# Kernel tuning notes

Measured on AMD Instinct MI355X. Metric: run time of the kernel, lower is better.

## Reference

```python
import jax, jax.numpy as jnp
import numpy as np

EPS = 1e-5


def _lstm_agg(x, nbr_idx, Wih, Whh, bih, bhh):
    # x: [N, D] node feats; nbr_idx: [N, K]; LSTM hidden size == D (DGL lstm aggregator)
    seq = x[nbr_idx]                     # [N, K, D] irregular gather
    N, K, D = seq.shape
    seq_t = jnp.swapaxes(seq, 0, 1)      # [K, N, D] time-major for scan

    def step(carry, xt):
        h, c = carry
        z = xt @ Wih.T + bih + h @ Whh.T + bhh   # [N, 4D]; torch gate order i,f,g,o
        i, f, g, o = jnp.split(z, 4, axis=-1)
        i = jax.nn.sigmoid(i)
        f = jax.nn.sigmoid(f)
        g = jnp.tanh(g)
        o = jax.nn.sigmoid(o)
        c = f * c + i * g
        h = o * jnp.tanh(c)
        return (h, c), None

    zero = jnp.zeros((N, D), seq.dtype)
    (h, _), _ = jax.lax.scan(step, (zero, zero), seq_t)
    return h                             # final hidden state = neighbor aggregate


def _sage_layer(x, nbr_idx, Wih, Whh, bih, bhh, Wself, bself, Wneigh):
    h_neigh = _lstm_agg(x, nbr_idx, Wih, Whh, bih, bhh)
    return x @ Wself.T + bself + h_neigh @ Wneigh.T


def _bn(x, gamma, beta):
    # BatchNorm1d in training mode: batch statistics over the node axis
    mu = jnp.mean(x, axis=0)
    var = jnp.var(x, axis=0)
    return (x - mu) * jax.lax.rsqrt(var + EPS) * gamma + beta


def setup_inputs() -> dict:
    key = jax.random.key(0)
    N, K, D_IN, D_H = 100000, 16, 128, 128
    ks = jax.random.split(key, 20)
    s = 0.05
    inp = {
        "in_feat": jax.random.normal(ks[0], (N, D_IN), jnp.float32),
        "nbr_idx": jax.random.randint(ks[1], (N, K), 0, N, jnp.int32),
        # layer 1 (in_feats=128 -> h_feats=128), LSTM hidden = in_feats
        "Wih1": jax.random.normal(ks[2], (4 * D_IN, D_IN), jnp.float32) * s,
        "Whh1": jax.random.normal(ks[3], (4 * D_IN, D_IN), jnp.float32) * s,
        "bih1": jnp.zeros((4 * D_IN,), jnp.float32),
        "bhh1": jnp.zeros((4 * D_IN,), jnp.float32),
        "Wself1": jax.random.normal(ks[4], (D_H, D_IN), jnp.float32) * s,
        "bself1": jnp.zeros((D_H,), jnp.float32),
        "Wneigh1": jax.random.normal(ks[5], (D_H, D_IN), jnp.float32) * s,
        "gamma1": jnp.ones((D_H,), jnp.float32),
        "beta1": jnp.zeros((D_H,), jnp.float32),
        # layer 2 (h_feats=128 -> h_feats=128)
        "Wih2": jax.random.normal(ks[6], (4 * D_H, D_H), jnp.float32) * s,
        "Whh2": jax.random.normal(ks[7], (4 * D_H, D_H), jnp.float32) * s,
        "bih2": jnp.zeros((4 * D_H,), jnp.float32),
        "bhh2": jnp.zeros((4 * D_H,), jnp.float32),
        "Wself2": jax.random.normal(ks[8], (D_H, D_H), jnp.float32) * s,
        "bself2": jnp.zeros((D_H,), jnp.float32),
        "Wneigh2": jax.random.normal(ks[9], (D_H, D_H), jnp.float32) * s,
        "gamma2": jnp.ones((D_H,), jnp.float32),
        "beta2": jnp.zeros((D_H,), jnp.float32),
    }
    return inp


def reference(in_feat, nbr_idx,
              Wih1, Whh1, bih1, bhh1, Wself1, bself1, Wneigh1, gamma1, beta1,
              Wih2, Whh2, bih2, bhh2, Wself2, bself2, Wneigh2, gamma2, beta2):
    h = _sage_layer(in_feat, nbr_idx, Wih1, Whh1, bih1, bhh1, Wself1, bself1, Wneigh1)
    h = jax.nn.relu(_bn(h, gamma1, beta1))
    h = _sage_layer(h, nbr_idx, Wih2, Whh2, bih2, bhh2, Wself2, bself2, Wneigh2)
    h = _bn(h, gamma2, beta2)
    return h
```

## Files before the change

### kernel.cpp

```cpp
#include <hip/hip_runtime.h>

typedef unsigned short u16;
typedef unsigned int u32;
typedef unsigned long long u64;
typedef __attribute__((ext_vector_type(8))) short short8;
typedef __attribute__((ext_vector_type(4))) float float4_t;

__device__ __forceinline__ float bf2f(u16 v) {
    union { u32 u; float f; } x; x.u = ((u32)v) << 16; return x.f;
}
__device__ __forceinline__ u16 f2bf(float f) {
    union { float f; u32 u; } x; x.f = f;
    u32 r = x.u + 0x7FFFu + ((x.u >> 16) & 1u);
    return (u16)(r >> 16);
}
__device__ __forceinline__ u32 pk2bf(float hi, float lo) {
    union { float f; u32 u; } a, b; a.f = hi; b.f = lo;
    return __builtin_amdgcn_perm(a.u + 0x8000u, b.u + 0x8000u, 0x07060302u);
}
#define LOG2E 1.44269504088896340736f
__device__ __forceinline__ float sigm(float x) {
    return __builtin_amdgcn_rcpf(1.f + __builtin_amdgcn_exp2f(-LOG2E * x));
}
__device__ __forceinline__ float tanh_(float x) {
    float t = __builtin_amdgcn_exp2f(2.f * LOG2E * x);
    return 1.f - 2.f * __builtin_amdgcn_rcpf(1.f + t);
}

__device__ __forceinline__ float4_t mfma16(short8 a, short8 b, float4_t c) {
    return __builtin_amdgcn_mfma_f32_16x16x32_bf16(a, b, c, 0, 0, 0);
}

__device__ __forceinline__ short8 ldfrag(const u16* p) { return *(const short8*)p; }
__device__ __forceinline__ short8 ldfrag(const float* p) {
    float4_t a = *(const float4_t*)p;
    float4_t b = *(const float4_t*)(p + 4);
    short8 r;
#pragma unroll
    for (int j = 0; j < 4; ++j) { r[j] = (short)f2bf(a[j]); r[4 + j] = (short)f2bf(b[j]); }
    return r;
}

template<typename AT>
__global__ __launch_bounds__(256) void gemm_ih(
    const AT* __restrict__ A, const float* __restrict__ W,
    const float* __restrict__ b1, const float* __restrict__ b2,
    u16* __restrict__ C, int M)
{
    const int P = 512;
    const int lane = threadIdx.x & 63;
    const int w    = threadIdx.x >> 6;
    const int l15  = lane & 15;
    const int quad = lane >> 4;
    const int rowbase = blockIdx.x * 64;
    const int colbase = blockIdx.y * 128 + w * 32;

    short8 af[4][4];
#pragma unroll
    for (int mb = 0; mb < 4; ++mb) {
        int row = rowbase + mb * 16 + l15;
        if (row >= M) row = M - 1;
        const AT* ap = A + (size_t)row * 128 + quad * 8;
#pragma unroll
        for (int kb = 0; kb < 4; ++kb) af[mb][kb] = ldfrag(ap + kb * 32);
    }
    short8 bfr[2][4];
#pragma unroll
    for (int nb = 0; nb < 2; ++nb) {
        int col = colbase + nb * 16 + l15;
        const float* wp = W + (size_t)col * 128 + quad * 8;
#pragma unroll
        for (int kb = 0; kb < 4; ++kb) bfr[nb][kb] = ldfrag(wp + kb * 32);
    }
    const float4_t z4 = {0.f, 0.f, 0.f, 0.f};
    float bias[2];
#pragma unroll
    for (int nb = 0; nb < 2; ++nb) {
        int col = colbase + nb * 16 + l15;
        bias[nb] = b1[col] + b2[col];
    }
#pragma unroll
    for (int mb = 0; mb < 4; ++mb)
#pragma unroll
        for (int nb = 0; nb < 2; ++nb) {
            float4_t a = z4;
#pragma unroll
            for (int kb = 0; kb < 4; ++kb) a = mfma16(af[mb][kb], bfr[nb][kb], a);
#pragma unroll
            for (int r = 0; r < 4; ++r) {
                int row = rowbase + mb * 16 + quad * 4 + r;
                int col = colbase + nb * 16 + l15;
                if (row < M) C[(size_t)row * P + col] = f2bf(a[r] + bias[nb]);
            }
        }
}

template<typename T>
__device__ __forceinline__ void accum_gemm(
    const T* __restrict__ A, const float* __restrict__ W,
    float4_t (&acc)[4][2], int M, int rowbase, int colbase, int l15, int quad)
{
    short8 af[4][4];
#pragma unroll
    for (int mb = 0; mb < 4; ++mb) {
        int row = rowbase + mb * 16 + l15;
        if (row >= M) row = M - 1;
        const T* ap = A + (size_t)row * 128 + quad * 8;
#pragma unroll
        for (int kb = 0; kb < 4; ++kb) af[mb][kb] = ldfrag(ap + kb * 32);
    }
    short8 bfr[2][4];
#pragma unroll
    for (int nb = 0; nb < 2; ++nb) {
        int col = colbase + nb * 16 + l15;
        const float* wp = W + (size_t)col * 128 + quad * 8;
#pragma unroll
        for (int kb = 0; kb < 4; ++kb) bfr[nb][kb] = ldfrag(wp + kb * 32);
    }
#pragma unroll
    for (int mb = 0; mb < 4; ++mb)
#pragma unroll
        for (int nb = 0; nb < 2; ++nb)
#pragma unroll
            for (int kb = 0; kb < 4; ++kb)
                acc[mb][nb] = mfma16(af[mb][kb], bfr[nb][kb], acc[mb][nb]);
}

template<typename AT2>
__global__ __launch_bounds__(256) void gemm_out(
    const u16* __restrict__ A1, const float* __restrict__ W1,
    const AT2* __restrict__ A2, const float* __restrict__ W2,
    const float* __restrict__ bias, float* __restrict__ C,
    float* __restrict__ stats, int M)
{
    const int P = 128;
    const int lane = threadIdx.x & 63;
    const int w    = threadIdx.x >> 6;
    const int l15  = lane & 15;
    const int quad = lane >> 4;
    const int rowbase = blockIdx.x * 64;
    const int colbase = w * 32;

    float4_t acc[4][2];
    const float4_t z4 = {0.f, 0.f, 0.f, 0.f};
#pragma unroll
    for (int mb = 0; mb < 4; ++mb)
#pragma unroll
        for (int nb = 0; nb < 2; ++nb) acc[mb][nb] = z4;

    accum_gemm(A1, W1, acc, M, rowbase, colbase, l15, quad);
    accum_gemm(A2, W2, acc, M, rowbase, colbase, l15, quad);

    float s[2] = {0.f, 0.f}, sq[2] = {0.f, 0.f};
#pragma unroll
    for (int nb = 0; nb < 2; ++nb) {
        int col = colbase + nb * 16 + l15;
        float bb = bias[col];
#pragma unroll
        for (int mb = 0; mb < 4; ++mb)
#pragma unroll
            for (int r = 0; r < 4; ++r) {
                int row = rowbase + mb * 16 + quad * 4 + r;
                if (row < M) {
                    float v = acc[mb][nb][r] + bb;
                    C[(size_t)row * P + col] = v;
                    s[nb] += v; sq[nb] += v * v;
                }
            }
    }
#pragma unroll
    for (int nb = 0; nb < 2; ++nb) {
        float t1 = s[nb], t2 = sq[nb];
        t1 += __shfl_xor(t1, 16); t1 += __shfl_xor(t1, 32);
        t2 += __shfl_xor(t2, 16); t2 += __shfl_xor(t2, 32);
        int col = colbase + nb * 16 + l15;
        if (quad == 0) atomicAdd(&stats[col], t1);
        if (quad == 1) atomicAdd(&stats[P + col], t2);
    }
}

__global__ __launch_bounds__(512, 2) void lstm_kernel(
    const u16* __restrict__ Xih,
    const int* __restrict__ nbr,
    const float* __restrict__ Whh,
    u16* __restrict__ Hout,
    int N)
{
    __shared__ u16 hbuf[2][64][136];
    __shared__ int nbrs[16][72];
    const int tid  = threadIdx.x;
    const int lane = tid & 63;
    const int w    = tid >> 6;
    const int l15  = lane & 15;
    const int quad = lane >> 4;
    const int base = blockIdx.x * 64;

    short8 whA[4][4];
#pragma unroll
    for (int g = 0; g < 4; ++g) {
        int row = 128 * g + 16 * w + l15;
        const float* wp = Whh + (size_t)row * 128 + quad * 8;
#pragma unroll
        for (int kb = 0; kb < 4; ++kb) whA[g][kb] = ldfrag(wp + kb * 32);
    }
    short8 I;
    {
        int off = (w & 1) ? 16 : 0;
#pragma unroll
        for (int j = 0; j < 8; ++j) {
            int k = quad * 8 + j;
            I[j] = (short)((k == l15 + off) ? 0x3F80 : 0);
        }
    }
    u32* hz = (u32*)&hbuf[0][0][0];
    for (int i = tid; i < 2 * 64 * 136 / 2; i += 512) hz[i] = 0u;
    for (int i = tid; i < 64 * 16; i += 512) {
        int node = base + (i >> 4);
        if (node >= N) node = N - 1;
        nbrs[i & 15][i >> 4] = nbr[(size_t)node * 16 + (i & 15)];
    }
    __syncthreads();

    const int xcol0 = 32 * (w >> 1);
    short8 xf[4][4];
#pragma unroll
    for (int nb = 0; nb < 4; ++nb) {
        int node = nbrs[0][l15 + 16 * nb];
        const u16* xp = Xih + (size_t)node * 512 + xcol0 + quad * 8;
#pragma unroll
        for (int g = 0; g < 4; ++g) xf[nb][g] = *(const short8*)(xp + 128 * g);
    }

    const float4_t z4 = {0.f, 0.f, 0.f, 0.f};
    float4_t c[4];
#pragma unroll
    for (int nb = 0; nb < 4; ++nb) c[nb] = z4;
    float4_t hlast[4];

    for (int t = 0; t < 16; ++t) {
        const int p = t & 1;
#pragma unroll
        for (int nb = 0; nb < 4; ++nb) {
            const u16* hp = &hbuf[p][l15 + 16 * nb][quad * 8];
            short8 hb[4];
#pragma unroll
            for (int kb = 0; kb < 4; ++kb) hb[kb] = *(const short8*)(hp + kb * 32);
            float4_t z[4];
#pragma unroll
            for (int g = 0; g < 4; ++g) z[g] = mfma16(I, xf[nb][g], z4);
            if (t < 15) {
                int node = nbrs[t + 1][l15 + 16 * nb];
                const u16* xp = Xih + (size_t)node * 512 + xcol0 + quad * 8;
#pragma unroll
                for (int g = 0; g < 4; ++g) xf[nb][g] = *(const short8*)(xp + 128 * g);
            }
#pragma unroll
            for (int g = 0; g < 4; ++g)
#pragma unroll
                for (int kb = 0; kb < 4; ++kb)
                    z[g] = mfma16(whA[g][kb], hb[kb], z[g]);
            float4_t hv;
#pragma unroll
            for (int r = 0; r < 4; ++r) {
                float i_ = sigm(z[0][r]);
                float f_ = sigm(z[1][r]);
                float g_ = tanh_(z[2][r]);
                float o_ = sigm(z[3][r]);
                float cc = f_ * c[nb][r] + i_ * g_;
                c[nb][r] = cc;
                hv[r] = o_ * tanh_(cc);
            }
            hlast[nb] = hv;
            u64 pkd = ((u64)pk2bf(hv[3], hv[2]) << 32) | pk2bf(hv[1], hv[0]);
            *(u64*)&hbuf[1 - p][l15 + 16 * nb][16 * w + quad * 4] = pkd;
        }
        __syncthreads();
    }
#pragma unroll
    for (int nb = 0; nb < 4; ++nb) {
        int row = base + l15 + 16 * nb;
        if (row < N) {
            u64 pkd = ((u64)pk2bf(hlast[nb][3], hlast[nb][2]) << 32)
                      | pk2bf(hlast[nb][1], hlast[nb][0]);
            *(u64*)(Hout + (size_t)row * 128 + 16 * w + quad * 4) = pkd;
        }
    }
}

__global__ void zero_stats(float* s) { s[threadIdx.x] = 0.f; }

__global__ void bn_prep(float* stats, const float* __restrict__ gamma,
                        const float* __restrict__ beta, float invN)
{
    int cidx = threadIdx.x;
    float s = stats[cidx], sq = stats[128 + cidx];
    float mu = s * invN;
    float var = sq * invN - mu * mu;
    float sc = gamma[cidx] * rsqrtf(var + 1e-5f);
    stats[256 + cidx] = sc;
    stats[384 + cidx] = beta[cidx] - mu * sc;
}

template<typename OT>
__global__ __launch_bounds__(256) void bn_apply(
    const float* __restrict__ X, const float* __restrict__ stats,
    OT* __restrict__ Y, int M, int relu)
{
    int gid = blockIdx.x * 256 + threadIdx.x;
    int row = gid >> 4;
    int cs  = (gid & 15) * 8;
    if (row >= M) return;
    float4_t a = *(const float4_t*)(X + (size_t)row * 128 + cs);
    float4_t b = *(const float4_t*)(X + (size_t)row * 128 + cs + 4);
    float v[8];
#pragma unroll
    for (int j = 0; j < 8; ++j) {
        float x = (j < 4) ? a[j] : b[j - 4];
        float t = x * stats[256 + cs + j] + stats[384 + cs + j];
        v[j] = relu ? fmaxf(t, 0.f) : t;
    }
    if constexpr (sizeof(OT) == 2) {
        short8 ov;
#pragma unroll
        for (int j = 0; j < 8; ++j) ov[j] = (short)f2bf(v[j]);
        *(short8*)((u16*)Y + (size_t)row * 128 + cs) = ov;
    } else {
        float4_t o1, o2;
#pragma unroll
        for (int j = 0; j < 4; ++j) { o1[j] = v[j]; o2[j] = v[4 + j]; }
        *(float4_t*)((float*)Y + (size_t)row * 128 + cs) = o1;
        *(float4_t*)((float*)Y + (size_t)row * 128 + cs + 4) = o2;
    }
}

extern "C" void kernel_launch(void* const* d_in, const int* in_sizes, int n_in,
                              void* d_out, int out_size, void* d_ws, size_t ws_size,
                              hipStream_t stream)
{
    const float* in_feat = (const float*)d_in[0];
    const int*   nbr     = (const int*)d_in[1];
    const float* Wih1 = (const float*)d_in[2];
    const float* Whh1 = (const float*)d_in[3];
    const float* bih1 = (const float*)d_in[4];
    const float* bhh1 = (const float*)d_in[5];
    const float* Wself1  = (const float*)d_in[6];
    const float* bself1  = (const float*)d_in[7];
    const float* Wneigh1 = (const float*)d_in[8];
    const float* gamma1  = (const float*)d_in[9];
    const float* beta1   = (const float*)d_in[10];
    const float* Wih2 = (const float*)d_in[11];
    const float* Whh2 = (const float*)d_in[12];
    const float* bih2 = (const float*)d_in[13];
    const float* bhh2 = (const float*)d_in[14];
    const float* Wself2  = (const float*)d_in[15];
    const float* bself2  = (const float*)d_in[16];
    const float* Wneigh2 = (const float*)d_in[17];
    const float* gamma2  = (const float*)d_in[18];
    const float* beta2   = (const float*)d_in[19];

    const int N = in_sizes[0] / 128;

    char* ws = (char*)d_ws;
    u16*   Xih   = (u16*)ws;
    float* Pbuf  = (float*)ws;
    u16*   hn    = (u16*)(ws + (size_t)N * 1024);
    float* stats = (float*)(ws + (size_t)N * 1024 + (size_t)N * 256);
    u16*   hcur  = (u16*)d_out;

    const int nblk = (N + 63) / 64;
    const float invN = 1.0f / (float)N;
    const int bnblk = (N * 16 + 255) / 256;

    zero_stats<<<dim3(1), dim3(256), 0, stream>>>(stats);
    gemm_ih<float><<<dim3(nblk, 4), dim3(256), 0, stream>>>(in_feat, Wih1, bih1, bhh1, Xih, N);
    lstm_kernel<<<dim3(nblk), dim3(512), 0, stream>>>(Xih, nbr, Whh1, hn, N);
    gemm_out<float><<<dim3(nblk, 1), dim3(256), 0, stream>>>(hn, Wneigh1, in_feat, Wself1,
                                                             bself1, Pbuf, stats, N);
    bn_prep<<<dim3(1), dim3(128), 0, stream>>>(stats, gamma1, beta1, invN);
    bn_apply<u16><<<dim3(bnblk), dim3(256), 0, stream>>>(Pbuf, stats, hcur, N, 1);

    zero_stats<<<dim3(1), dim3(256), 0, stream>>>(stats);
    gemm_ih<u16><<<dim3(nblk, 4), dim3(256), 0, stream>>>(hcur, Wih2, bih2, bhh2, Xih, N);
    lstm_kernel<<<dim3(nblk), dim3(512), 0, stream>>>(Xih, nbr, Whh2, hn, N);
    gemm_out<u16><<<dim3(nblk, 1), dim3(256), 0, stream>>>(hn, Wneigh2, hcur, Wself2,
                                                           bself2, Pbuf, stats, N);
    bn_prep<<<dim3(1), dim3(128), 0, stream>>>(stats, gamma2, beta2, invN);
    bn_apply<float><<<dim3(bnblk), dim3(256), 0, stream>>>(Pbuf, stats, (float*)d_out, N, 0);
}
```

Measured before the change: 1.680 ms.

## Prescale gate pre-activations, drop identity MFMA, swizzle LSTM hidden-state LDS

Folds the sigmoid/tanh exponent scale factors (-log2e, 2log2e) into the input-projection GEMM output and into the recurrent weights, so the LSTM cell calls exp2 directly without a multiply. The precomputed input contribution is now loaded in the MFMA output layout (4 bf16 per lane) and unpacked into the accumulator, which replaces the identity-matrix MFMA that used to transpose it. The padded hidden-state LDS buffer becomes an XOR-swizzled unpadded one to avoid bank conflicts. The launch bound now asks for 4 blocks per SM, which may force register spills. Storing bf16 values after scaling changes rounding slightly.

```diff
diff --git a/kernel.cpp b/kernel.cpp
--- a/kernel.cpp
+++ b/kernel.cpp
@@ -5,6 +5,7 @@
 typedef unsigned long long u64;
 typedef __attribute__((ext_vector_type(8))) short short8;
 typedef __attribute__((ext_vector_type(4))) float float4_t;
+typedef __attribute__((ext_vector_type(2))) u32 u32x2;
 
 __device__ __forceinline__ float bf2f(u16 v) {
     union { u32 u; float f; } x; x.u = ((u32)v) << 16; return x.f;
@@ -14,14 +15,14 @@
     u32 r = x.u + 0x7FFFu + ((x.u >> 16) & 1u);
     return (u16)(r >> 16);
 }
+__device__ __forceinline__ float bitsf(u32 u) {
+    union { u32 u; float f; } x; x.u = u; return x.f;
+}
 __device__ __forceinline__ u32 pk2bf(float hi, float lo) {
     union { float f; u32 u; } a, b; a.f = hi; b.f = lo;
     return __builtin_amdgcn_perm(a.u + 0x8000u, b.u + 0x8000u, 0x07060302u);
 }
 #define LOG2E 1.44269504088896340736f
-__device__ __forceinline__ float sigm(float x) {
-    return __builtin_amdgcn_rcpf(1.f + __builtin_amdgcn_exp2f(-LOG2E * x));
-}
 __device__ __forceinline__ float tanh_(float x) {
     float t = __builtin_amdgcn_exp2f(2.f * LOG2E * x);
     return 1.f - 2.f * __builtin_amdgcn_rcpf(1.f + t);
@@ -38,6 +39,14 @@
     short8 r;
 #pragma unroll
     for (int j = 0; j < 4; ++j) { r[j] = (short)f2bf(a[j]); r[4 + j] = (short)f2bf(b[j]); }
+    return r;
+}
+__device__ __forceinline__ short8 ldfrag_scaled(const float* p, float s) {
+    float4_t a = *(const float4_t*)p;
+    float4_t b = *(const float4_t*)(p + 4);
+    short8 r;
+#pragma unroll
+    for (int j = 0; j < 4; ++j) { r[j] = (short)f2bf(a[j] * s); r[4 + j] = (short)f2bf(b[j] * s); }
     return r;
 }
 
@@ -73,11 +82,12 @@
         for (int kb = 0; kb < 4; ++kb) bfr[nb][kb] = ldfrag(wp + kb * 32);
     }
     const float4_t z4 = {0.f, 0.f, 0.f, 0.f};
-    float bias[2];
+    float bias[2], scl[2];
 #pragma unroll
     for (int nb = 0; nb < 2; ++nb) {
         int col = colbase + nb * 16 + l15;
         bias[nb] = b1[col] + b2[col];
+        scl[nb] = (col >= 256 && col < 384) ? (2.f * LOG2E) : (-LOG2E);
     }
 #pragma unroll
     for (int mb = 0; mb < 4; ++mb)
@@ -90,7 +100,7 @@
             for (int r = 0; r < 4; ++r) {
                 int row = rowbase + mb * 16 + quad * 4 + r;
                 int col = colbase + nb * 16 + l15;
-                if (row < M) C[(size_t)row * P + col] = f2bf(a[r] + bias[nb]);
+                if (row < M) C[(size_t)row * P + col] = f2bf((a[r] + bias[nb]) * scl[nb]);
             }
         }
 }
@@ -179,14 +189,14 @@
     }
 }
 
-__global__ __launch_bounds__(512, 2) void lstm_kernel(
+__global__ __launch_bounds__(512, 4) void lstm_kernel(
     const u16* __restrict__ Xih,
     const int* __restrict__ nbr,
     const float* __restrict__ Whh,
     u16* __restrict__ Hout,
     int N)
 {
-    __shared__ u16 hbuf[2][64][136];
+    __shared__ u16 hbuf[2][64][128];
     __shared__ int nbrs[16][72];
     const int tid  = threadIdx.x;
     const int lane = tid & 63;
@@ -199,21 +209,13 @@
 #pragma unroll
     for (int g = 0; g < 4; ++g) {
         int row = 128 * g + 16 * w + l15;
+        float s = (g == 2) ? (2.f * LOG2E) : (-LOG2E);
         const float* wp = Whh + (size_t)row * 128 + quad * 8;
 #pragma unroll
-        for (int kb = 0; kb < 4; ++kb) whA[g][kb] = ldfrag(wp + kb * 32);
-    }
-    short8 I;
-    {
-        int off = (w & 1) ? 16 : 0;
-#pragma unroll
-        for (int j = 0; j < 8; ++j) {
-            int k = quad * 8 + j;
-            I[j] = (short)((k == l15 + off) ? 0x3F80 : 0);
-        }
+        for (int kb = 0; kb < 4; ++kb) whA[g][kb] = ldfrag_scaled(wp + kb * 32, s);
     }
     u32* hz = (u32*)&hbuf[0][0][0];
-    for (int i = tid; i < 2 * 64 * 136 / 2; i += 512) hz[i] = 0u;
+    for (int i = tid; i < 2 * 64 * 128 / 2; i += 512) hz[i] = 0u;
     for (int i = tid; i < 64 * 16; i += 512) {
         int node = base + (i >> 4);
         if (node >= N) node = N - 1;
@@ -221,38 +223,47 @@
     }
     __syncthreads();
 
-    const int xcol0 = 32 * (w >> 1);
-    short8 xf[4][4];
+    const int xoff = 16 * w + 4 * quad;
+
+    u32x2 xfu[4][4];
 #pragma unroll
     for (int nb = 0; nb < 4; ++nb) {
         int node = nbrs[0][l15 + 16 * nb];
-        const u16* xp = Xih + (size_t)node * 512 + xcol0 + quad * 8;
-#pragma unroll
-        for (int g = 0; g < 4; ++g) xf[nb][g] = *(const short8*)(xp + 128 * g);
+        const u16* xp = Xih + (size_t)node * 512 + xoff;
+#pragma unroll
+        for (int g = 0; g < 4; ++g) xfu[nb][g] = *(const u32x2*)(xp + 128 * g);
     }
 
     const float4_t z4 = {0.f, 0.f, 0.f, 0.f};
     float4_t c[4];
 #pragma unroll
     for (int nb = 0; nb < 4; ++nb) c[nb] = z4;
-    float4_t hlast[4];
+    u64 pklast[4];
 
     for (int t = 0; t < 16; ++t) {
         const int p = t & 1;
 #pragma unroll
         for (int nb = 0; nb < 4; ++nb) {
-            const u16* hp = &hbuf[p][l15 + 16 * nb][quad * 8];
+            const int row = l15 + 16 * nb;
+            const char* hrow = (const char*)&hbuf[p][row][0];
             short8 hb[4];
 #pragma unroll
-            for (int kb = 0; kb < 4; ++kb) hb[kb] = *(const short8*)(hp + kb * 32);
+            for (int kb = 0; kb < 4; ++kb) {
+                int ch = (quad + 4 * kb) ^ (row & 7);
+                hb[kb] = *(const short8*)(hrow + (ch << 4));
+            }
             float4_t z[4];
 #pragma unroll
-            for (int g = 0; g < 4; ++g) z[g] = mfma16(I, xf[nb][g], z4);
+            for (int g = 0; g < 4; ++g) {
+                u32 w0 = xfu[nb][g][0], w1 = xfu[nb][g][1];
+                z[g][0] = bitsf(w0 << 16); z[g][1] = bitsf(w0 & 0xFFFF0000u);
+                z[g][2] = bitsf(w1 << 16); z[g][3] = bitsf(w1 & 0xFFFF0000u);
+            }
             if (t < 15) {
                 int node = nbrs[t + 1][l15 + 16 * nb];
-                const u16* xp = Xih + (size_t)node * 512 + xcol0 + quad * 8;
-#pragma unroll
-                for (int g = 0; g < 4; ++g) xf[nb][g] = *(const short8*)(xp + 128 * g);
+                const u16* xp = Xih + (size_t)node * 512 + xoff;
+#pragma unroll
+                for (int g = 0; g < 4; ++g) xfu[nb][g] = *(const u32x2*)(xp + 128 * g);
             }
 #pragma unroll
             for (int g = 0; g < 4; ++g)
@@ -262,28 +273,27 @@
             float4_t hv;
 #pragma unroll
             for (int r = 0; r < 4; ++r) {
-                float i_ = sigm(z[0][r]);
-                float f_ = sigm(z[1][r]);
-                float g_ = tanh_(z[2][r]);
-                float o_ = sigm(z[3][r]);
+                float i_ = __builtin_amdgcn_rcpf(1.f + __builtin_amdgcn_exp2f(z[0][r]));
+                float f_ = __builtin_amdgcn_rcpf(1.f + __builtin_amdgcn_exp2f(z[1][r]));
+                float g_ = 1.f - 2.f * __builtin_amdgcn_rcpf(1.f + __builtin_amdgcn_exp2f(z[2][r]));
+                float o_ = __builtin_amdgcn_rcpf(1.f + __builtin_amdgcn_exp2f(z[3][r]));
                 float cc = f_ * c[nb][r] + i_ * g_;
                 c[nb][r] = cc;
                 hv[r] = o_ * tanh_(cc);
             }
-            hlast[nb] = hv;
             u64 pkd = ((u64)pk2bf(hv[3], hv[2]) << 32) | pk2bf(hv[1], hv[0]);
-            *(u64*)&hbuf[1 - p][l15 + 16 * nb][16 * w + quad * 4] = pkd;
+            pklast[nb] = pkd;
+            int ch = (2 * w + (quad >> 1)) ^ (row & 7);
+            int sw = (ch << 4) | ((quad & 1) << 3);
+            *(u64*)((char*)&hbuf[1 - p][row][0] + sw) = pkd;
         }
         __syncthreads();
     }
 #pragma unroll
     for (int nb = 0; nb < 4; ++nb) {
         int row = base + l15 + 16 * nb;
-        if (row < N) {
-            u64 pkd = ((u64)pk2bf(hlast[nb][3], hlast[nb][2]) << 32)
-                      | pk2bf(hlast[nb][1], hlast[nb][0]);
-            *(u64*)(Hout + (size_t)row * 128 + 16 * w + quad * 4) = pkd;
-        }
+        if (row < N)
+            *(u64*)(Hout + (size_t)row * 128 + 16 * w + 4 * quad) = pklast[nb];
     }
 }
 
```

Measured after the change: 2.273 ms. 35.2% more time.
